# Kernel tuning notes

Measured on AMD Instinct MI355X. Metric: run time of the kernel, lower is better.

The kernel has to match this reference:

```python
import jax, jax.numpy as jnp
import numpy as np

LAYER_SIZES = [1024, 1024, 1024, 1024, 1024, 1024, 512]
MAX_PATHS = 128
BATCH = 128
N_LAYERS = len(LAYER_SIZES) - 1


def setup_inputs() -> dict:
    key = jax.random.key(0)
    keys = jax.random.split(key, 1 + 2 * N_LAYERS)
    inp = {"x": jax.random.normal(keys[0], (BATCH, LAYER_SIZES[0]), dtype=jnp.float32)}
    for i in range(N_LAYERS):
        inp[f"W{i}"] = jax.random.normal(keys[1 + 2 * i], (LAYER_SIZES[i], LAYER_SIZES[i + 1]), dtype=jnp.float32) * 0.01
        inp[f"b{i}"] = jax.random.normal(keys[2 + 2 * i], (LAYER_SIZES[i + 1],), dtype=jnp.float32) * 0.01
    return inp


def _layer(data, W, b):
    # data: [B, in_feat, P] -> [B, out_feat, 3P]
    B, _, P = data.shape
    O = W.shape[1]
    pos = jnp.einsum('bfp,fo->bpo', data, W) + b          # [B, P, O]; neg branch is exactly -pos
    branches = jnp.stack([-pos, jnp.zeros_like(pos), pos], axis=-1)  # [B, P, O, 3]
    # transpose(1,2) then reshape: interleave branches per source path, matching torch
    return branches.transpose(0, 2, 1, 3).reshape(B, O, P * 3)


def _prune(data, keep):
    # keep top-`keep` paths by L2 norm over the feature dim
    norms = jnp.linalg.norm(data, axis=1)                 # [B, P]
    _, idx = jax.lax.top_k(norms, keep)                   # [B, keep]
    return jnp.take_along_axis(data, idx[:, None, :], axis=-1)


def _forward(x, Ws, bs):
    data = x[:, :, None]                                   # [B, F, 1]
    for i in range(N_LAYERS):
        data = _layer(data, Ws[i], bs[i])
        if i < N_LAYERS - 1:
            data = jnp.tanh(data)
        if data.shape[-1] > MAX_PATHS:
            data = _prune(data, MAX_PATHS)
    # collapse with 'max_abs': per (batch, feature) pick path with largest |value|
    idx = jnp.argmax(jnp.abs(data), axis=-1, keepdims=True)
    output = jnp.take_along_axis(data, idx, axis=-1).squeeze(-1)
    return output, data


def reference(x, W0, b0, W1, b1, W2, b2, W3, b3, W4, b4, W5, b5):
    Ws = [W0, W1, W2, W3, W4, W5]
    bs = [b0, b1, b2, b3, b4, b5]
    return _forward(x, Ws, bs)
```

## Files before the change

### kernel.cpp

```cpp
#include <hip/hip_runtime.h>
#include <math.h>


using s8v = __attribute__((ext_vector_type(8))) short;
using f4v = __attribute__((ext_vector_type(4))) float;

__device__ __forceinline__ float bf2f(short b) {
  unsigned u = ((unsigned)(unsigned short)b) << 16;
  return __builtin_bit_cast(float, u);
}
__device__ __forceinline__ short f2bf(float f) {
  unsigned u = __builtin_bit_cast(unsigned, f);
  u = (u + 0x7FFFu + ((u >> 16) & 1u)) >> 16;
  return (short)u;
}
__device__ __forceinline__ void split_store(float f, short* hi, short* lo) {
  short h = f2bf(f);
  *hi = h;
  *lo = f2bf(f - bf2f(h));
}

struct TWArgs {
  const float* W[6];
  short* Th[6];
  short* Tl[6];
};
__global__ void __launch_bounds__(256)
transW_all(TWArgs a, const float* __restrict__ x, short* __restrict__ A0h,
           short* __restrict__ A0l) {
  __shared__ float tile[64][65];
  const int t = threadIdx.x;
  if (blockIdx.z == 6) {
    const int bf = blockIdx.y * 16 + blockIdx.x;
    if (bf < 128) {
      int i = (bf * 256 + t) * 4;
      float4 v = *(const float4*)&x[i];
      short4 h, l;
      h.x = f2bf(v.x); l.x = f2bf(v.x - bf2f(h.x));
      h.y = f2bf(v.y); l.y = f2bf(v.y - bf2f(h.y));
      h.z = f2bf(v.z); l.z = f2bf(v.z - bf2f(h.z));
      h.w = f2bf(v.w); l.w = f2bf(v.w - bf2f(h.w));
      *(short4*)&A0h[i] = h;
      *(short4*)&A0l[i] = l;
    }
    return;
  }
  const int z = blockIdx.z;
  const int N = (z == 5) ? 512 : 1024;
  const int n0 = blockIdx.x * 64, k0 = blockIdx.y * 64;
  if (n0 >= N) return;
  const float* __restrict__ W = a.W[z];
  short* __restrict__ Th = a.Th[z];
  short* __restrict__ Tl = a.Tl[z];
  const int r = t >> 4, c4 = (t & 15) * 4;
#pragma unroll
  for (int i = 0; i < 4; ++i) {
    int rr = r + 16 * i;
    float4 v = *(const float4*)&W[(size_t)(k0 + rr) * N + n0 + c4];
    tile[rr][c4 + 0] = v.x;
    tile[rr][c4 + 1] = v.y;
    tile[rr][c4 + 2] = v.z;
    tile[rr][c4 + 3] = v.w;
  }
  __syncthreads();
#pragma unroll
  for (int i = 0; i < 4; ++i) {
    int n = r + 16 * i;
    short4 h, l;
    float f0 = tile[c4 + 0][n], f1 = tile[c4 + 1][n];
    float f2 = tile[c4 + 2][n], f3 = tile[c4 + 3][n];
    h.x = f2bf(f0); l.x = f2bf(f0 - bf2f(h.x));
    h.y = f2bf(f1); l.y = f2bf(f1 - bf2f(h.y));
    h.z = f2bf(f2); l.z = f2bf(f2 - bf2f(h.z));
    h.w = f2bf(f3); l.w = f2bf(f3 - bf2f(h.w));
    size_t o = (size_t)(n0 + n) * 1024 + k0 + c4;
    *(short4*)&Th[o] = h;
    *(short4*)&Tl[o] = l;
  }
}

template <int MODE, int D, int KS>
__global__ void __launch_bounds__(256, 2)
mfma_gemm(const short* __restrict__ Ah, const short* __restrict__ Al,
          const short* __restrict__ Bh, const short* __restrict__ Bl,
          const float* __restrict__ bias, short* __restrict__ Oh,
          short* __restrict__ Ol, float* __restrict__ Of, int N, int Dn) {
  constexpr int KC = 1024 / KS;
  constexpr int BKP = 40;
  __shared__ short As_h[64 * BKP], As_l[64 * BKP];
  __shared__ short Bs_h[64 * BKP], Bs_l[64 * BKP];
  const int t = threadIdx.x;
  const int row0 = blockIdx.y * 64;
  const int col0 = blockIdx.x * 64;
  const int kb = blockIdx.z * KC;
  const int sr = t >> 2, sko = (t & 3) * 8;
  const short* Ahp = Ah + (size_t)(row0 + sr) * 1024 + kb + sko;
  const short* Alp = Al + (size_t)(row0 + sr) * 1024 + kb + sko;
  const short* Bhp = Bh + (size_t)(col0 + sr) * 1024 + kb + sko;
  const short* Blp = Bl + (size_t)(col0 + sr) * 1024 + kb + sko;
  const int w = t >> 6, lane = t & 63;
  const int l16 = lane & 15, q = lane >> 4;
  const int wm0 = (w & 1) * 32, wn0 = (w >> 1) * 32;
  const int abase = (wm0 + l16) * BKP + q * 8;
  const int bbase = (wn0 + l16) * BKP + q * 8;
  f4v acc[2][2];
#pragma unroll
  for (int i = 0; i < 2; ++i)
#pragma unroll
    for (int j = 0; j < 2; ++j) acc[i][j] = (f4v){0.f, 0.f, 0.f, 0.f};
  uint4 rah = *(const uint4*)(Ahp);
  uint4 ral = *(const uint4*)(Alp);
  uint4 rbh = *(const uint4*)(Bhp);
  uint4 rbl = *(const uint4*)(Blp);
  for (int k0 = 0; k0 < KC; k0 += 32) {
    __syncthreads();
    *(uint4*)&As_h[sr * BKP + sko] = rah;
    *(uint4*)&As_l[sr * BKP + sko] = ral;
    *(uint4*)&Bs_h[sr * BKP + sko] = rbh;
    *(uint4*)&Bs_l[sr * BKP + sko] = rbl;
    if (k0 + 32 < KC) {
      rah = *(const uint4*)(Ahp + k0 + 32);
      ral = *(const uint4*)(Alp + k0 + 32);
      rbh = *(const uint4*)(Bhp + k0 + 32);
      rbl = *(const uint4*)(Blp + k0 + 32);
    }
    __syncthreads();
    s8v ah[2], al[2], bh[2], bl[2];
#pragma unroll
    for (int mt = 0; mt < 2; ++mt) {
      ah[mt] = *(const s8v*)&As_h[abase + mt * 16 * BKP];
      al[mt] = *(const s8v*)&As_l[abase + mt * 16 * BKP];
    }
#pragma unroll
    for (int nt = 0; nt < 2; ++nt) {
      bh[nt] = *(const s8v*)&Bs_h[bbase + nt * 16 * BKP];
      bl[nt] = *(const s8v*)&Bs_l[bbase + nt * 16 * BKP];
    }
#pragma unroll
    for (int mt = 0; mt < 2; ++mt)
#pragma unroll
      for (int nt = 0; nt < 2; ++nt) {
        acc[mt][nt] = __builtin_amdgcn_mfma_f32_16x16x32_bf16(
            ah[mt], bh[nt], acc[mt][nt], 0, 0, 0);
        acc[mt][nt] = __builtin_amdgcn_mfma_f32_16x16x32_bf16(
            ah[mt], bl[nt], acc[mt][nt], 0, 0, 0);
        acc[mt][nt] = __builtin_amdgcn_mfma_f32_16x16x32_bf16(
            al[mt], bh[nt], acc[mt][nt], 0, 0, 0);
      }
  }
  const int R = (int)gridDim.y << 6;
#pragma unroll
  for (int nt = 0; nt < 2; ++nt) {
    int gcol = col0 + wn0 + nt * 16 + l16;
    float bc = (MODE == 1) ? bias[gcol] : 0.f;
#pragma unroll
    for (int mt = 0; mt < 2; ++mt) {
#pragma unroll
      for (int r = 0; r < 4; ++r) {
        float v = acc[mt][nt][r];
        int rr = row0 + wm0 + mt * 16 + q * 4 + r;
        if (MODE == 1) {
          int b = rr / D, u = rr - b * D;
          size_t ob = (size_t)(b * Dn) * N + gcol;
          size_t om = ob + (size_t)(1 + 2 * u) * N;
          size_t op = ob + (size_t)(2 + 2 * u) * N;
          split_store(tanhf(bc - v), &Oh[om], &Ol[om]);
          split_store(tanhf(bc + v), &Oh[op], &Ol[op]);
          if (u == 0) split_store(tanhf(bc), &Oh[ob], &Ol[ob]);
        } else if (MODE == 2) {
          Of[(size_t)rr * N + gcol] = v;
        } else {
          Of[((size_t)blockIdx.z * R + rr) * N + gcol] = v;
        }
      }
    }
  }
}

template <int KS>
__global__ void __launch_bounds__(256)
comb0_hl(const float* __restrict__ P, const float* __restrict__ bias,
         short* __restrict__ Oh, short* __restrict__ Ol, int R, int N) {
  int i = blockIdx.x * 256 + threadIdx.x;
  int n4 = N >> 2;
  int r = i / n4, c4 = (i - r * n4) * 4;
  float4 y = *(const float4*)&P[(size_t)r * N + c4];
  size_t stride = (size_t)R * N;
#pragma unroll
  for (int ks = 1; ks < KS; ++ks) {
    const float4 p = *(const float4*)&P[ks * stride + (size_t)r * N + c4];
    y.x += p.x; y.y += p.y; y.z += p.z; y.w += p.w;
  }
  float4 bc = *(const float4*)(bias + c4);
  float t0 = tanhf(bc.x + y.x), t1 = tanhf(bc.y + y.y);
  float t2 = tanhf(bc.z + y.z), t3 = tanhf(bc.w + y.w);
  short4 h, l;
  h.x = f2bf(t0); l.x = f2bf(t0 - bf2f(h.x));
  h.y = f2bf(t1); l.y = f2bf(t1 - bf2f(h.y));
  h.z = f2bf(t2); l.z = f2bf(t2 - bf2f(h.z));
  h.w = f2bf(t3); l.w = f2bf(t3 - bf2f(h.w));
  *(short4*)&Oh[(size_t)r * N + c4] = h;
  *(short4*)&Ol[(size_t)r * N + c4] = l;
}

template <int KS, int D>
__global__ void __launch_bounds__(256)
comb1_hl(const float* __restrict__ P, const float* __restrict__ bias,
         short* __restrict__ Oh, short* __restrict__ Ol, int R, int N,
         int Dn) {
  int i = blockIdx.x * 256 + threadIdx.x;
  int n4 = N >> 2;
  int r = i / n4, c4 = (i - r * n4) * 4;
  int b = r / D, u = r - b * D;
  float4 y = *(const float4*)&P[(size_t)r * N + c4];
  size_t stride = (size_t)R * N;
#pragma unroll
  for (int ks = 1; ks < KS; ++ks) {
    const float4 p = *(const float4*)&P[ks * stride + (size_t)r * N + c4];
    y.x += p.x; y.y += p.y; y.z += p.z; y.w += p.w;
  }
  float4 bc = *(const float4*)(bias + c4);
  size_t ob = (size_t)(b * Dn) * N + c4;
  size_t om = ob + (size_t)(1 + 2 * u) * N;
  size_t op = ob + (size_t)(2 + 2 * u) * N;
  {
    float t0 = tanhf(bc.x - y.x), t1 = tanhf(bc.y - y.y);
    float t2 = tanhf(bc.z - y.z), t3 = tanhf(bc.w - y.w);
    short4 h, l;
    h.x = f2bf(t0); l.x = f2bf(t0 - bf2f(h.x));
    h.y = f2bf(t1); l.y = f2bf(t1 - bf2f(h.y));
    h.z = f2bf(t2); l.z = f2bf(t2 - bf2f(h.z));
    h.w = f2bf(t3); l.w = f2bf(t3 - bf2f(h.w));
    *(short4*)&Oh[om] = h;
    *(short4*)&Ol[om] = l;
  }
  {
    float t0 = tanhf(bc.x + y.x), t1 = tanhf(bc.y + y.y);
    float t2 = tanhf(bc.z + y.z), t3 = tanhf(bc.w + y.w);
    short4 h, l;
    h.x = f2bf(t0); l.x = f2bf(t0 - bf2f(h.x));
    h.y = f2bf(t1); l.y = f2bf(t1 - bf2f(h.y));
    h.z = f2bf(t2); l.z = f2bf(t2 - bf2f(h.z));
    h.w = f2bf(t3); l.w = f2bf(t3 - bf2f(h.w));
    *(short4*)&Oh[op] = h;
    *(short4*)&Ol[op] = l;
  }
  if (u == 0) {
    float t0 = tanhf(bc.x), t1 = tanhf(bc.y);
    float t2 = tanhf(bc.z), t3 = tanhf(bc.w);
    short4 h, l;
    h.x = f2bf(t0); l.x = f2bf(t0 - bf2f(h.x));
    h.y = f2bf(t1); l.y = f2bf(t1 - bf2f(h.y));
    h.z = f2bf(t2); l.z = f2bf(t2 - bf2f(h.z));
    h.w = f2bf(t3); l.w = f2bf(t3 - bf2f(h.w));
    *(short4*)&Oh[ob] = h;
    *(short4*)&Ol[ob] = l;
  }
}

__global__ void __launch_bounds__(256)
rownorm_hl(const short* __restrict__ hi, const short* __restrict__ lo,
           float* __restrict__ ns) {
  int row = blockIdx.x;
  int t = threadIdx.x;
  size_t base = (size_t)row * 1024 + t * 4;
  short4 h = *(const short4*)&hi[base];
  short4 l = *(const short4*)&lo[base];
  float v0 = bf2f(h.x) + bf2f(l.x);
  float v1 = bf2f(h.y) + bf2f(l.y);
  float v2 = bf2f(h.z) + bf2f(l.z);
  float v3 = bf2f(h.w) + bf2f(l.w);
  float s = v0 * v0 + v1 * v1 + v2 * v2 + v3 * v3;
  __shared__ float red[256];
  red[t] = s;
  __syncthreads();
  for (int off = 128; off; off >>= 1) {
    if (t < off) red[t] += red[t + off];
    __syncthreads();
  }
  if (t == 0) ns[row] = red[0];
}

__global__ void __launch_bounds__(256)
stats5_k(const float* __restrict__ Y5, const float* __restrict__ b5,
         float* __restrict__ dotv, float* __restrict__ nrmv) {
  int row = blockIdx.x;
  int t = threadIdx.x;
  __shared__ float rd[256], rn[256];
  const float* y = Y5 + (size_t)row * 512;
  float d = 0.f, n2 = 0.f;
  for (int o = t; o < 512; o += 256) {
    float v = y[o];
    d = fmaf(b5[o], v, d);
    n2 = fmaf(v, v, n2);
  }
  rd[t] = d;
  rn[t] = n2;
  __syncthreads();
  for (int off = 128; off; off >>= 1) {
    if (t < off) {
      rd[t] += rd[t + off];
      rn[t] += rn[t + off];
    }
    __syncthreads();
  }
  if (t == 0) {
    dotv[row] = rd[0];
    nrmv[row] = rn[0];
  }
}

__global__ void __launch_bounds__(384)
prune45_k(const float* __restrict__ ns, const float* __restrict__ dotv,
          const float* __restrict__ nrmv, const float* __restrict__ b5,
          int* __restrict__ kept4, int* __restrict__ kept5) {
  const int b = blockIdx.x, t = threadIdx.x;
  __shared__ float nss[31];
  __shared__ float rb[256];
  __shared__ float keyA[243];
  __shared__ int cls[243];
  __shared__ int k4s[128];
  __shared__ float pns[128];
  __shared__ float keyB[384];
  if (t < 31) nss[t] = ns[b * 31 + t];
  if (t < 256) {
    float a = b5[t], c = b5[t + 256];
    rb[t] = fmaf(a, a, 0.f);
    rb[t] = fmaf(c, c, rb[t]);
  }
  __syncthreads();
  for (int off = 128; off; off >>= 1) {
    if (t < off) rb[t] += rb[t + off];
    __syncthreads();
  }
  const float nb5 = rb[0];
  if (t < 243) {
    int j = t / 3, t4 = t - 3 * j;
    int d0 = j / 27, d1 = (j / 9) % 3, d2 = (j / 3) % 3, d3 = j % 3;
    int u = 0;
    u = (d0 == 1) ? 0 : (1 + 2 * u + (d0 == 2));
    u = (d1 == 1) ? 0 : (1 + 2 * u + (d1 == 2));
    u = (d2 == 1) ? 0 : (1 + 2 * u + (d2 == 2));
    u = (d3 == 1) ? 0 : (1 + 2 * u + (d3 == 2));
    cls[t] = u;
    keyA[t] = (t4 == 1) ? 0.f : nss[u];
  }
  __syncthreads();
  if (t < 243) {
    float k = keyA[t];
    int rank = 0;
    for (int e = 0; e < 243; ++e) {
      float ke = keyA[e];
      rank += (ke > k) || (ke == k && e < t);
    }
    if (rank < 128) {
      int t4 = t - 3 * (t / 3);
      int kv = (cls[t] << 1) | (t4 == 2 ? 1 : 0);
      k4s[rank] = kv;
      kept4[b * 128 + rank] = kv;
    }
  }
  __syncthreads();
  if (t < 128) {
    int k4 = k4s[t];
    int c = k4 >> 1;
    float s = (k4 & 1) ? 1.f : -1.f;
    pns[t] = nb5 + nrmv[b * 31 + c] + s * 2.f * dotv[b * 31 + c];
  }
  __syncthreads();
  const int m = t / 3, tt = t - 3 * m;
  keyB[t] = (tt == 1) ? 0.f : pns[m];
  __syncthreads();
  float k = keyB[t];
  int rank = 0;
  for (int e = 0; e < 384; ++e) {
    float ke = keyB[e];
    rank += (ke > k) || (ke == k && e < t);
  }
  if (rank < 128) kept5[b * 128 + rank] = (m << 1) | (tt == 2 ? 1 : 0);
}

__global__ void __launch_bounds__(256)
finalize_k(const float* __restrict__ Y5, const float* __restrict__ b5,
           const int* __restrict__ kept4, const int* __restrict__ kept5,
           float* __restrict__ out, float* __restrict__ dataout) {
  const int b = blockIdx.y;
  const int o0 = blockIdx.x * 64;
  __shared__ float Ys[31][65];
  __shared__ float bias_s[64];
  __shared__ float vt[64][130];
  __shared__ float ra[64][4];
  __shared__ float rv[64][4];
  const int t = threadIdx.x;
  for (int idx = t; idx < 31 * 64; idx += 256) {
    int c = idx >> 6, o = idx & 63;
    Ys[c][o] = Y5[((size_t)b * 31 + c) * 512 + o0 + o];
  }
  if (t < 64) bias_s[t] = b5[o0 + t];
  const int rr = t & 127, oh = t >> 7;
  int k5 = kept5[b * 128 + rr];
  int m = k5 >> 1;
  float sig = (k5 & 1) ? 1.f : -1.f;
  int k4 = kept4[b * 128 + m];
  int cc = k4 >> 1;
  float s4 = (k4 & 1) ? 1.f : -1.f;
  float afac = sig * s4;
  __syncthreads();
#pragma unroll
  for (int ol = 0; ol < 32; ++ol) {
    int o = oh * 32 + ol;
    float v = sig * bias_s[o] + afac * Ys[cc][o];
    dataout[((size_t)b * 512 + o0 + o) * 128 + rr] = v;
    vt[o][rr] = v;
  }
  __syncthreads();
  int o = t >> 2, q = t & 3;
  float bestv = vt[o][q * 32];
  float besta = fabsf(bestv);
  for (int i = 1; i < 32; ++i) {
    float v = vt[o][q * 32 + i];
    float a = fabsf(v);
    if (a > besta) {
      besta = a;
      bestv = v;
    }
  }
  ra[o][q] = besta;
  rv[o][q] = bestv;
  __syncthreads();
  if (t < 64) {
    float ba = ra[t][0], bv = rv[t][0];
#pragma unroll
    for (int qq = 1; qq < 4; ++qq) {
      if (ra[t][qq] > ba) {
        ba = ra[t][qq];
        bv = rv[t][qq];
      }
    }
    out[(size_t)b * 512 + o0 + t] = bv;
  }
}

extern "C" void kernel_launch(void* const* d_in, const int* in_sizes, int n_in,
                              void* d_out, int out_size, void* d_ws,
                              size_t ws_size, hipStream_t stream) {
  const float* x = (const float*)d_in[0];
  const float* Wt[6];
  const float* bs[6];
  for (int i = 0; i < 6; ++i) {
    Wt[i] = (const float*)d_in[1 + 2 * i];
    bs[i] = (const float*)d_in[2 + 2 * i];
  }
  char* base = (char*)d_ws;
  short* A0h = (short*)(base + 0);
  short* A0l = (short*)(base + 262144);
  short* Wh[6], *Wl[6];
  {
    size_t off = 524288;
    for (int i = 0; i < 6; ++i) {
      size_t sz = (i < 5) ? 2097152 : 1048576;
      Wh[i] = (short*)(base + off);
      Wl[i] = (short*)(base + off + sz);
      off += 2 * sz;
    }
  }
  short* C1h = (short*)(base + 23592960), *C1l = (short*)(base + 23855104);
  short* C2h = (short*)(base + 24117248), *C2l = (short*)(base + 24903680);
  short* C3h = (short*)(base + 25690112), *C3l = (short*)(base + 27525120);
  short* C4h = (short*)(base + 29360128), *C4l = (short*)(base + 33292288);
  short* C5h = (short*)(base + 524288);
  short* C5l = (short*)(base + 8912896);
  float* PA = (float*)(base + 29360128);
  float* PB = (float*)(base + 524288);
  float* Y5 = (float*)(base + 23592960);
  float* ns = (float*)(base + 37224448);
  float* dotv = (float*)(base + 37240320);
  float* nrmv = (float*)(base + 37256192);
  int* kept4 = (int*)(base + 37272068);
  int* kept5 = (int*)(base + 37337604);
  float* outp = (float*)d_out;
  float* dataout = outp + 128 * 512;

  dim3 blk(256);
  TWArgs twa;
  for (int i = 0; i < 6; ++i) {
    twa.W[i] = Wt[i];
    twa.Th[i] = Wh[i];
    twa.Tl[i] = Wl[i];
  }
  transW_all<<<dim3(16, 16, 7), blk, 0, stream>>>(twa, x, A0h, A0l);
  mfma_gemm<3, 1, 4><<<dim3(16, 2, 4), blk, 0, stream>>>(
      A0h, A0l, Wh[0], Wl[0], nullptr, nullptr, nullptr, PA, 1024, 0);
  comb0_hl<4><<<dim3(128), blk, 0, stream>>>(PA, bs[0], C1h, C1l, 128, 1024);
  mfma_gemm<3, 1, 4><<<dim3(16, 2, 4), blk, 0, stream>>>(
      C1h, C1l, Wh[1], Wl[1], nullptr, nullptr, nullptr, PA, 1024, 0);
  comb1_hl<4, 1><<<dim3(128), blk, 0, stream>>>(PA, bs[1], C2h, C2l, 128, 1024,
                                                3);
  mfma_gemm<3, 3, 4><<<dim3(16, 6, 4), blk, 0, stream>>>(
      C2h, C2l, Wh[2], Wl[2], nullptr, nullptr, nullptr, PA, 1024, 0);
  comb1_hl<4, 3><<<dim3(384), blk, 0, stream>>>(PA, bs[2], C3h, C3l, 384, 1024,
                                                7);
  mfma_gemm<3, 7, 2><<<dim3(16, 14, 2), blk, 0, stream>>>(
      C3h, C3l, Wh[3], Wl[3], nullptr, nullptr, nullptr, PB, 1024, 0);
  comb1_hl<2, 7><<<dim3(896), blk, 0, stream>>>(PB, bs[3], C4h, C4l, 896, 1024,
                                                15);
  mfma_gemm<1, 15, 1><<<dim3(16, 30), blk, 0, stream>>>(
      C4h, C4l, Wh[4], Wl[4], bs[4], C5h, C5l, nullptr, 1024, 31);
  rownorm_hl<<<dim3(3968), blk, 0, stream>>>(C5h, C5l, ns);
  mfma_gemm<2, 31, 1><<<dim3(8, 62), blk, 0, stream>>>(
      C5h, C5l, Wh[5], Wl[5], nullptr, nullptr, nullptr, Y5, 512, 0);
  stats5_k<<<dim3(3968), blk, 0, stream>>>(Y5, bs[5], dotv, nrmv);
  prune45_k<<<dim3(128), dim3(384), 0, stream>>>(ns, dotv, nrmv, bs[5], kept4,
                                                 kept5);
  finalize_k<<<dim3(8, 128), blk, 0, stream>>>(Y5, bs[5], kept4, kept5, outp,
                                               dataout);
}
```

Before: 238.5 us.

## Double GEMM K-step to 64 and fuse layer-5 GEMM with row-norm kernel

The MFMA GEMM now stages 64 K-elements per shared-memory iteration instead of 32 (padded row stride raised to 72), which halves the number of barrier pairs per K loop but doubles register prefetch and LDS footprint. The GEMM body is factored into a device function so the final-layer GEMM and the row-norm reduction can run as one launch. Blocks below 496 do the GEMM and the rest compute row norms, which removes a kernel launch and lets the two independent jobs overlap. The larger LDS use per block may lower occupancy, and the row-norm blocks now inherit the GEMM's launch bounds and shared-memory allocation.

```diff
diff --git a/kernel.cpp b/kernel.cpp
--- a/kernel.cpp
+++ b/kernel.cpp
@@ -80,19 +80,20 @@
 }
 
 template <int MODE, int D, int KS>
-__global__ void __launch_bounds__(256, 2)
-mfma_gemm(const short* __restrict__ Ah, const short* __restrict__ Al,
-          const short* __restrict__ Bh, const short* __restrict__ Bl,
-          const float* __restrict__ bias, short* __restrict__ Oh,
-          short* __restrict__ Ol, float* __restrict__ Of, int N, int Dn) {
+__device__ __forceinline__ void gemm_body(
+    int bx, int by, int bz, int R, const short* __restrict__ Ah,
+    const short* __restrict__ Al, const short* __restrict__ Bh,
+    const short* __restrict__ Bl, const float* __restrict__ bias,
+    short* __restrict__ Oh, short* __restrict__ Ol, float* __restrict__ Of,
+    int N, int Dn) {
   constexpr int KC = 1024 / KS;
-  constexpr int BKP = 40;
+  constexpr int BKP = 72;
   __shared__ short As_h[64 * BKP], As_l[64 * BKP];
   __shared__ short Bs_h[64 * BKP], Bs_l[64 * BKP];
   const int t = threadIdx.x;
-  const int row0 = blockIdx.y * 64;
-  const int col0 = blockIdx.x * 64;
-  const int kb = blockIdx.z * KC;
+  const int row0 = by * 64;
+  const int col0 = bx * 64;
+  const int kb = bz * KC;
   const int sr = t >> 2, sko = (t & 3) * 8;
   const short* Ahp = Ah + (size_t)(row0 + sr) * 1024 + kb + sko;
   const short* Alp = Al + (size_t)(row0 + sr) * 1024 + kb + sko;
@@ -108,47 +109,59 @@
   for (int i = 0; i < 2; ++i)
 #pragma unroll
     for (int j = 0; j < 2; ++j) acc[i][j] = (f4v){0.f, 0.f, 0.f, 0.f};
-  uint4 rah = *(const uint4*)(Ahp);
-  uint4 ral = *(const uint4*)(Alp);
-  uint4 rbh = *(const uint4*)(Bhp);
-  uint4 rbl = *(const uint4*)(Blp);
-  for (int k0 = 0; k0 < KC; k0 += 32) {
+  uint4 rah[2], ral[2], rbh[2], rbl[2];
+#pragma unroll
+  for (int c = 0; c < 2; ++c) {
+    rah[c] = *(const uint4*)(Ahp + c * 32);
+    ral[c] = *(const uint4*)(Alp + c * 32);
+    rbh[c] = *(const uint4*)(Bhp + c * 32);
+    rbl[c] = *(const uint4*)(Blp + c * 32);
+  }
+  for (int k0 = 0; k0 < KC; k0 += 64) {
     __syncthreads();
-    *(uint4*)&As_h[sr * BKP + sko] = rah;
-    *(uint4*)&As_l[sr * BKP + sko] = ral;
-    *(uint4*)&Bs_h[sr * BKP + sko] = rbh;
-    *(uint4*)&Bs_l[sr * BKP + sko] = rbl;
-    if (k0 + 32 < KC) {
-      rah = *(const uint4*)(Ahp + k0 + 32);
-      ral = *(const uint4*)(Alp + k0 + 32);
-      rbh = *(const uint4*)(Bhp + k0 + 32);
-      rbl = *(const uint4*)(Blp + k0 + 32);
+#pragma unroll
+    for (int c = 0; c < 2; ++c) {
+      *(uint4*)&As_h[sr * BKP + sko + c * 32] = rah[c];
+      *(uint4*)&As_l[sr * BKP + sko + c * 32] = ral[c];
+      *(uint4*)&Bs_h[sr * BKP + sko + c * 32] = rbh[c];
+      *(uint4*)&Bs_l[sr * BKP + sko + c * 32] = rbl[c];
+    }
+    if (k0 + 64 < KC) {
+#pragma unroll
+      for (int c = 0; c < 2; ++c) {
+        rah[c] = *(const uint4*)(Ahp + k0 + 64 + c * 32);
+        ral[c] = *(const uint4*)(Alp + k0 + 64 + c * 32);
+        rbh[c] = *(const uint4*)(Bhp + k0 + 64 + c * 32);
+        rbl[c] = *(const uint4*)(Blp + k0 + 64 + c * 32);
+      }
     }
     __syncthreads();
-    s8v ah[2], al[2], bh[2], bl[2];
-#pragma unroll
-    for (int mt = 0; mt < 2; ++mt) {
-      ah[mt] = *(const s8v*)&As_h[abase + mt * 16 * BKP];
-      al[mt] = *(const s8v*)&As_l[abase + mt * 16 * BKP];
-    }
-#pragma unroll
-    for (int nt = 0; nt < 2; ++nt) {
-      bh[nt] = *(const s8v*)&Bs_h[bbase + nt * 16 * BKP];
-      bl[nt] = *(const s8v*)&Bs_l[bbase + nt * 16 * BKP];
-    }
-#pragma unroll
-    for (int mt = 0; mt < 2; ++mt)
+#pragma unroll
+    for (int kk = 0; kk < 64; kk += 32) {
+      s8v ah[2], al[2], bh[2], bl[2];
+#pragma unroll
+      for (int mt = 0; mt < 2; ++mt) {
+        ah[mt] = *(const s8v*)&As_h[abase + mt * 16 * BKP + kk];
+        al[mt] = *(const s8v*)&As_l[abase + mt * 16 * BKP + kk];
+      }
 #pragma unroll
       for (int nt = 0; nt < 2; ++nt) {
-        acc[mt][nt] = __builtin_amdgcn_mfma_f32_16x16x32_bf16(
-            ah[mt], bh[nt], acc[mt][nt], 0, 0, 0);
-        acc[mt][nt] = __builtin_amdgcn_mfma_f32_16x16x32_bf16(
-            ah[mt], bl[nt], acc[mt][nt], 0, 0, 0);
-        acc[mt][nt] = __builtin_amdgcn_mfma_f32_16x16x32_bf16(
-            al[mt], bh[nt], acc[mt][nt], 0, 0, 0);
+        bh[nt] = *(const s8v*)&Bs_h[bbase + nt * 16 * BKP + kk];
+        bl[nt] = *(const s8v*)&Bs_l[bbase + nt * 16 * BKP + kk];
       }
-  }
-  const int R = (int)gridDim.y << 6;
+#pragma unroll
+      for (int mt = 0; mt < 2; ++mt)
+#pragma unroll
+        for (int nt = 0; nt < 2; ++nt) {
+          acc[mt][nt] = __builtin_amdgcn_mfma_f32_16x16x32_bf16(
+              ah[mt], bh[nt], acc[mt][nt], 0, 0, 0);
+          acc[mt][nt] = __builtin_amdgcn_mfma_f32_16x16x32_bf16(
+              ah[mt], bl[nt], acc[mt][nt], 0, 0, 0);
+          acc[mt][nt] = __builtin_amdgcn_mfma_f32_16x16x32_bf16(
+              al[mt], bh[nt], acc[mt][nt], 0, 0, 0);
+        }
+    }
+  }
 #pragma unroll
   for (int nt = 0; nt < 2; ++nt) {
     int gcol = col0 + wn0 + nt * 16 + l16;
@@ -170,10 +183,56 @@
         } else if (MODE == 2) {
           Of[(size_t)rr * N + gcol] = v;
         } else {
-          Of[((size_t)blockIdx.z * R + rr) * N + gcol] = v;
+          Of[((size_t)bz * R + rr) * N + gcol] = v;
         }
       }
     }
+  }
+}
+
+template <int MODE, int D, int KS>
+__global__ void __launch_bounds__(256, 2)
+mfma_gemm(const short* __restrict__ Ah, const short* __restrict__ Al,
+          const short* __restrict__ Bh, const short* __restrict__ Bl,
+          const float* __restrict__ bias, short* __restrict__ Oh,
+          short* __restrict__ Ol, float* __restrict__ Of, int N, int Dn) {
+  gemm_body<MODE, D, KS>(blockIdx.x, blockIdx.y, blockIdx.z,
+                         (int)gridDim.y << 6, Ah, Al, Bh, Bl, bias, Oh, Ol,
+                         Of, N, Dn);
+}
+
+__device__ __forceinline__ void rownorm_body(const short* __restrict__ hi,
+                                             const short* __restrict__ lo,
+                                             float* __restrict__ ns, int row) {
+  int t = threadIdx.x;
+  size_t base = (size_t)row * 1024 + t * 4;
+  short4 h = *(const short4*)&hi[base];
+  short4 l = *(const short4*)&lo[base];
+  float v0 = bf2f(h.x) + bf2f(l.x);
+  float v1 = bf2f(h.y) + bf2f(l.y);
+  float v2 = bf2f(h.z) + bf2f(l.z);
+  float v3 = bf2f(h.w) + bf2f(l.w);
+  float s = v0 * v0 + v1 * v1 + v2 * v2 + v3 * v3;
+  __shared__ float red[256];
+  red[t] = s;
+  __syncthreads();
+  for (int off = 128; off; off >>= 1) {
+    if (t < off) red[t] += red[t + off];
+    __syncthreads();
+  }
+  if (t == 0) ns[row] = red[0];
+}
+
+__global__ void __launch_bounds__(256, 2)
+gemm5_rownorm(const short* __restrict__ C5h, const short* __restrict__ C5l,
+              const short* __restrict__ W5h, const short* __restrict__ W5l,
+              float* __restrict__ Y5, float* __restrict__ ns) {
+  const int bid = blockIdx.x;
+  if (bid < 496) {
+    gemm_body<2, 31, 1>(bid & 7, bid >> 3, 0, 0, C5h, C5l, W5h, W5l, nullptr,
+                        nullptr, nullptr, Y5, 512, 0);
+  } else {
+    rownorm_body(C5h, C5l, ns, bid - 496);
   }
 }
 
@@ -256,29 +315,6 @@
     *(short4*)&Oh[ob] = h;
     *(short4*)&Ol[ob] = l;
   }
-}
-
-__global__ void __launch_bounds__(256)
-rownorm_hl(const short* __restrict__ hi, const short* __restrict__ lo,
-           float* __restrict__ ns) {
-  int row = blockIdx.x;
-  int t = threadIdx.x;
-  size_t base = (size_t)row * 1024 + t * 4;
-  short4 h = *(const short4*)&hi[base];
-  short4 l = *(const short4*)&lo[base];
-  float v0 = bf2f(h.x) + bf2f(l.x);
-  float v1 = bf2f(h.y) + bf2f(l.y);
-  float v2 = bf2f(h.z) + bf2f(l.z);
-  float v3 = bf2f(h.w) + bf2f(l.w);
-  float s = v0 * v0 + v1 * v1 + v2 * v2 + v3 * v3;
-  __shared__ float red[256];
-  red[t] = s;
-  __syncthreads();
-  for (int off = 128; off; off >>= 1) {
-    if (t < off) red[t] += red[t + off];
-    __syncthreads();
-  }
-  if (t == 0) ns[row] = red[0];
 }
 
 __global__ void __launch_bounds__(256)
@@ -506,9 +542,8 @@
                                                 15);
   mfma_gemm<1, 15, 1><<<dim3(16, 30), blk, 0, stream>>>(
       C4h, C4l, Wh[4], Wl[4], bs[4], C5h, C5l, nullptr, 1024, 31);
-  rownorm_hl<<<dim3(3968), blk, 0, stream>>>(C5h, C5l, ns);
-  mfma_gemm<2, 31, 1><<<dim3(8, 62), blk, 0, stream>>>(
-      C5h, C5l, Wh[5], Wl[5], nullptr, nullptr, nullptr, Y5, 512, 0);
+  gemm5_rownorm<<<dim3(496 + 3968), blk, 0, stream>>>(C5h, C5l, Wh[5], Wl[5],
+                                                      Y5, ns);
   stats5_k<<<dim3(3968), blk, 0, stream>>>(Y5, bs[5], dotv, nrmv);
   prune45_k<<<dim3(128), dim3(384), 0, stream>>>(ns, dotv, nrmv, bs[5], kept4,
                                                  kept5);
```

After: 397.2 us. +66.5%, slower.

## Halve GEMM row tile to 32 and fuse final GEMM with row-norm kernel

Applied to the files above, without the earlier changes.

Shrinks the MFMA GEMM block tile from 64x64 to 32x64, so each wave computes a 32x16 strip. Grid y-dimensions double, giving more blocks for these small-M GEMMs to fill the CUs. A-tile loading is split so half the threads load the hi part and half the lo part. The last GEMM and the row-norm reduction are merged into one launch that branches on block id, which removes a launch and lets the two independent jobs run concurrently. The cost is less B-tile reuse per block and more total global traffic for B.

```diff
diff --git a/kernel.cpp b/kernel.cpp
--- a/kernel.cpp
+++ b/kernel.cpp
@@ -80,85 +80,76 @@
 }
 
 template <int MODE, int D, int KS>
-__global__ void __launch_bounds__(256, 2)
-mfma_gemm(const short* __restrict__ Ah, const short* __restrict__ Al,
-          const short* __restrict__ Bh, const short* __restrict__ Bl,
-          const float* __restrict__ bias, short* __restrict__ Oh,
-          short* __restrict__ Ol, float* __restrict__ Of, int N, int Dn) {
+__device__ __forceinline__ void gemm_body(
+    int bx, int by, int bz, int R, const short* __restrict__ Ah,
+    const short* __restrict__ Al, const short* __restrict__ Bh,
+    const short* __restrict__ Bl, const float* __restrict__ bias,
+    short* __restrict__ Oh, short* __restrict__ Ol, float* __restrict__ Of,
+    int N, int Dn) {
   constexpr int KC = 1024 / KS;
   constexpr int BKP = 40;
-  __shared__ short As_h[64 * BKP], As_l[64 * BKP];
+  __shared__ short As_h[32 * BKP], As_l[32 * BKP];
   __shared__ short Bs_h[64 * BKP], Bs_l[64 * BKP];
   const int t = threadIdx.x;
-  const int row0 = blockIdx.y * 64;
-  const int col0 = blockIdx.x * 64;
-  const int kb = blockIdx.z * KC;
+  const int row0 = by * 32;
+  const int col0 = bx * 64;
+  const int kb = bz * KC;
   const int sr = t >> 2, sko = (t & 3) * 8;
-  const short* Ahp = Ah + (size_t)(row0 + sr) * 1024 + kb + sko;
-  const short* Alp = Al + (size_t)(row0 + sr) * 1024 + kb + sko;
   const short* Bhp = Bh + (size_t)(col0 + sr) * 1024 + kb + sko;
   const short* Blp = Bl + (size_t)(col0 + sr) * 1024 + kb + sko;
+  const int ta = t & 127;
+  const int ar = ta >> 2, ako = (ta & 3) * 8;
+  const short* Ap = (t < 128 ? Ah : Al) + (size_t)(row0 + ar) * 1024 + kb + ako;
+  short* AsDst = (t < 128) ? As_h : As_l;
   const int w = t >> 6, lane = t & 63;
   const int l16 = lane & 15, q = lane >> 4;
-  const int wm0 = (w & 1) * 32, wn0 = (w >> 1) * 32;
-  const int abase = (wm0 + l16) * BKP + q * 8;
+  const int wn0 = w * 16;
+  const int abase = l16 * BKP + q * 8;
   const int bbase = (wn0 + l16) * BKP + q * 8;
-  f4v acc[2][2];
-#pragma unroll
-  for (int i = 0; i < 2; ++i)
-#pragma unroll
-    for (int j = 0; j < 2; ++j) acc[i][j] = (f4v){0.f, 0.f, 0.f, 0.f};
-  uint4 rah = *(const uint4*)(Ahp);
-  uint4 ral = *(const uint4*)(Alp);
+  f4v acc[2];
+#pragma unroll
+  for (int i = 0; i < 2; ++i) acc[i] = (f4v){0.f, 0.f, 0.f, 0.f};
+  uint4 ra = *(const uint4*)(Ap);
   uint4 rbh = *(const uint4*)(Bhp);
   uint4 rbl = *(const uint4*)(Blp);
   for (int k0 = 0; k0 < KC; k0 += 32) {
     __syncthreads();
-    *(uint4*)&As_h[sr * BKP + sko] = rah;
-    *(uint4*)&As_l[sr * BKP + sko] = ral;
+    *(uint4*)&AsDst[ar * BKP + ako] = ra;
     *(uint4*)&Bs_h[sr * BKP + sko] = rbh;
     *(uint4*)&Bs_l[sr * BKP + sko] = rbl;
     if (k0 + 32 < KC) {
-      rah = *(const uint4*)(Ahp + k0 + 32);
-      ral = *(const uint4*)(Alp + k0 + 32);
+      ra = *(const uint4*)(Ap + k0 + 32);
       rbh = *(const uint4*)(Bhp + k0 + 32);
       rbl = *(const uint4*)(Blp + k0 + 32);
     }
     __syncthreads();
-    s8v ah[2], al[2], bh[2], bl[2];
+    s8v ah[2], al[2], bh, bl;
 #pragma unroll
     for (int mt = 0; mt < 2; ++mt) {
       ah[mt] = *(const s8v*)&As_h[abase + mt * 16 * BKP];
       al[mt] = *(const s8v*)&As_l[abase + mt * 16 * BKP];
     }
-#pragma unroll
-    for (int nt = 0; nt < 2; ++nt) {
-      bh[nt] = *(const s8v*)&Bs_h[bbase + nt * 16 * BKP];
-      bl[nt] = *(const s8v*)&Bs_l[bbase + nt * 16 * BKP];
-    }
-#pragma unroll
-    for (int mt = 0; mt < 2; ++mt)
-#pragma unroll
-      for (int nt = 0; nt < 2; ++nt) {
-        acc[mt][nt] = __builtin_amdgcn_mfma_f32_16x16x32_bf16(
-            ah[mt], bh[nt], acc[mt][nt], 0, 0, 0);
-        acc[mt][nt] = __builtin_amdgcn_mfma_f32_16x16x32_bf16(
-            ah[mt], bl[nt], acc[mt][nt], 0, 0, 0);
-        acc[mt][nt] = __builtin_amdgcn_mfma_f32_16x16x32_bf16(
-            al[mt], bh[nt], acc[mt][nt], 0, 0, 0);
-      }
-  }
-  const int R = (int)gridDim.y << 6;
-#pragma unroll
-  for (int nt = 0; nt < 2; ++nt) {
-    int gcol = col0 + wn0 + nt * 16 + l16;
+    bh = *(const s8v*)&Bs_h[bbase];
+    bl = *(const s8v*)&Bs_l[bbase];
+#pragma unroll
+    for (int mt = 0; mt < 2; ++mt) {
+      acc[mt] = __builtin_amdgcn_mfma_f32_16x16x32_bf16(ah[mt], bh, acc[mt],
+                                                        0, 0, 0);
+      acc[mt] = __builtin_amdgcn_mfma_f32_16x16x32_bf16(ah[mt], bl, acc[mt],
+                                                        0, 0, 0);
+      acc[mt] = __builtin_amdgcn_mfma_f32_16x16x32_bf16(al[mt], bh, acc[mt],
+                                                        0, 0, 0);
+    }
+  }
+  {
+    int gcol = col0 + wn0 + l16;
     float bc = (MODE == 1) ? bias[gcol] : 0.f;
 #pragma unroll
     for (int mt = 0; mt < 2; ++mt) {
 #pragma unroll
       for (int r = 0; r < 4; ++r) {
-        float v = acc[mt][nt][r];
-        int rr = row0 + wm0 + mt * 16 + q * 4 + r;
+        float v = acc[mt][r];
+        int rr = row0 + mt * 16 + q * 4 + r;
         if (MODE == 1) {
           int b = rr / D, u = rr - b * D;
           size_t ob = (size_t)(b * Dn) * N + gcol;
@@ -170,10 +161,56 @@
         } else if (MODE == 2) {
           Of[(size_t)rr * N + gcol] = v;
         } else {
-          Of[((size_t)blockIdx.z * R + rr) * N + gcol] = v;
+          Of[((size_t)bz * R + rr) * N + gcol] = v;
         }
       }
     }
+  }
+}
+
+template <int MODE, int D, int KS>
+__global__ void __launch_bounds__(256, 2)
+mfma_gemm(const short* __restrict__ Ah, const short* __restrict__ Al,
+          const short* __restrict__ Bh, const short* __restrict__ Bl,
+          const float* __restrict__ bias, short* __restrict__ Oh,
+          short* __restrict__ Ol, float* __restrict__ Of, int N, int Dn) {
+  gemm_body<MODE, D, KS>(blockIdx.x, blockIdx.y, blockIdx.z,
+                         (int)gridDim.y << 5, Ah, Al, Bh, Bl, bias, Oh, Ol,
+                         Of, N, Dn);
+}
+
+__device__ __forceinline__ void rownorm_body(const short* __restrict__ hi,
+                                             const short* __restrict__ lo,
+                                             float* __restrict__ ns, int row) {
+  int t = threadIdx.x;
+  size_t base = (size_t)row * 1024 + t * 4;
+  short4 h = *(const short4*)&hi[base];
+  short4 l = *(const short4*)&lo[base];
+  float v0 = bf2f(h.x) + bf2f(l.x);
+  float v1 = bf2f(h.y) + bf2f(l.y);
+  float v2 = bf2f(h.z) + bf2f(l.z);
+  float v3 = bf2f(h.w) + bf2f(l.w);
+  float s = v0 * v0 + v1 * v1 + v2 * v2 + v3 * v3;
+  __shared__ float red[256];
+  red[t] = s;
+  __syncthreads();
+  for (int off = 128; off; off >>= 1) {
+    if (t < off) red[t] += red[t + off];
+    __syncthreads();
+  }
+  if (t == 0) ns[row] = red[0];
+}
+
+__global__ void __launch_bounds__(256, 2)
+gemm5_rownorm(const short* __restrict__ C5h, const short* __restrict__ C5l,
+              const short* __restrict__ W5h, const short* __restrict__ W5l,
+              float* __restrict__ Y5, float* __restrict__ ns) {
+  const int bid = blockIdx.x;
+  if (bid < 992) {
+    gemm_body<2, 31, 1>(bid & 7, bid >> 3, 0, 0, C5h, C5l, W5h, W5l, nullptr,
+                        nullptr, nullptr, Y5, 512, 0);
+  } else {
+    rownorm_body(C5h, C5l, ns, bid - 992);
   }
 }
 
@@ -256,29 +293,6 @@
     *(short4*)&Oh[ob] = h;
     *(short4*)&Ol[ob] = l;
   }
-}
-
-__global__ void __launch_bounds__(256)
-rownorm_hl(const short* __restrict__ hi, const short* __restrict__ lo,
-           float* __restrict__ ns) {
-  int row = blockIdx.x;
-  int t = threadIdx.x;
-  size_t base = (size_t)row * 1024 + t * 4;
-  short4 h = *(const short4*)&hi[base];
-  short4 l = *(const short4*)&lo[base];
-  float v0 = bf2f(h.x) + bf2f(l.x);
-  float v1 = bf2f(h.y) + bf2f(l.y);
-  float v2 = bf2f(h.z) + bf2f(l.z);
-  float v3 = bf2f(h.w) + bf2f(l.w);
-  float s = v0 * v0 + v1 * v1 + v2 * v2 + v3 * v3;
-  __shared__ float red[256];
-  red[t] = s;
-  __syncthreads();
-  for (int off = 128; off; off >>= 1) {
-    if (t < off) red[t] += red[t + off];
-    __syncthreads();
-  }
-  if (t == 0) ns[row] = red[0];
 }
 
 __global__ void __launch_bounds__(256)
@@ -489,26 +503,25 @@
     twa.Tl[i] = Wl[i];
   }
   transW_all<<<dim3(16, 16, 7), blk, 0, stream>>>(twa, x, A0h, A0l);
-  mfma_gemm<3, 1, 4><<<dim3(16, 2, 4), blk, 0, stream>>>(
+  mfma_gemm<3, 1, 4><<<dim3(16, 4, 4), blk, 0, stream>>>(
       A0h, A0l, Wh[0], Wl[0], nullptr, nullptr, nullptr, PA, 1024, 0);
   comb0_hl<4><<<dim3(128), blk, 0, stream>>>(PA, bs[0], C1h, C1l, 128, 1024);
-  mfma_gemm<3, 1, 4><<<dim3(16, 2, 4), blk, 0, stream>>>(
+  mfma_gemm<3, 1, 4><<<dim3(16, 4, 4), blk, 0, stream>>>(
       C1h, C1l, Wh[1], Wl[1], nullptr, nullptr, nullptr, PA, 1024, 0);
   comb1_hl<4, 1><<<dim3(128), blk, 0, stream>>>(PA, bs[1], C2h, C2l, 128, 1024,
                                                 3);
-  mfma_gemm<3, 3, 4><<<dim3(16, 6, 4), blk, 0, stream>>>(
+  mfma_gemm<3, 3, 4><<<dim3(16, 12, 4), blk, 0, stream>>>(
       C2h, C2l, Wh[2], Wl[2], nullptr, nullptr, nullptr, PA, 1024, 0);
   comb1_hl<4, 3><<<dim3(384), blk, 0, stream>>>(PA, bs[2], C3h, C3l, 384, 1024,
                                                 7);
-  mfma_gemm<3, 7, 2><<<dim3(16, 14, 2), blk, 0, stream>>>(
+  mfma_gemm<3, 7, 2><<<dim3(16, 28, 2), blk, 0, stream>>>(
       C3h, C3l, Wh[3], Wl[3], nullptr, nullptr, nullptr, PB, 1024, 0);
   comb1_hl<2, 7><<<dim3(896), blk, 0, stream>>>(PB, bs[3], C4h, C4l, 896, 1024,
                                                 15);
-  mfma_gemm<1, 15, 1><<<dim3(16, 30), blk, 0, stream>>>(
+  mfma_gemm<1, 15, 1><<<dim3(16, 60), blk, 0, stream>>>(
       C4h, C4l, Wh[4], Wl[4], bs[4], C5h, C5l, nullptr, 1024, 31);
-  rownorm_hl<<<dim3(3968), blk, 0, stream>>>(C5h, C5l, ns);
-  mfma_gemm<2, 31, 1><<<dim3(8, 62), blk, 0, stream>>>(
-      C5h, C5l, Wh[5], Wl[5], nullptr, nullptr, nullptr, Y5, 512, 0);
+  gemm5_rownorm<<<dim3(992 + 3968), blk, 0, stream>>>(C5h, C5l, Wh[5], Wl[5],
+                                                      Y5, ns);
   stats5_k<<<dim3(3968), blk, 0, stream>>>(Y5, bs[5], dotv, nrmv);
   prune45_k<<<dim3(128), dim3(384), 0, stream>>>(ns, dotv, nrmv, bs[5], kept4,
                                                  kept5);
```

Result: slower. 251.2 us (+5.3%).

## Fuse rownorm into last GEMM launch and merge prune into finalize

Applied to the files above, without the earlier changes.

The row-norm kernel now runs as extra blocks in the same launch as the final GEMM, so the two independent jobs share one launch. The prune kernel is folded into finalize: each finalize block recomputes the top-k selection for its batch in shared memory instead of reading kept indices from global memory. This removes two launches and a global round-trip, but the prune work is now repeated by all 8 column blocks per batch, and finalize runs 384 threads with more shared memory.

```diff
diff --git a/kernel.cpp b/kernel.cpp
--- a/kernel.cpp
+++ b/kernel.cpp
@@ -80,19 +80,20 @@
 }
 
 template <int MODE, int D, int KS>
-__global__ void __launch_bounds__(256, 2)
-mfma_gemm(const short* __restrict__ Ah, const short* __restrict__ Al,
-          const short* __restrict__ Bh, const short* __restrict__ Bl,
-          const float* __restrict__ bias, short* __restrict__ Oh,
-          short* __restrict__ Ol, float* __restrict__ Of, int N, int Dn) {
+__device__ __forceinline__ void gemm_body(
+    int bx, int by, int bz, int R, const short* __restrict__ Ah,
+    const short* __restrict__ Al, const short* __restrict__ Bh,
+    const short* __restrict__ Bl, const float* __restrict__ bias,
+    short* __restrict__ Oh, short* __restrict__ Ol, float* __restrict__ Of,
+    int N, int Dn) {
   constexpr int KC = 1024 / KS;
   constexpr int BKP = 40;
   __shared__ short As_h[64 * BKP], As_l[64 * BKP];
   __shared__ short Bs_h[64 * BKP], Bs_l[64 * BKP];
   const int t = threadIdx.x;
-  const int row0 = blockIdx.y * 64;
-  const int col0 = blockIdx.x * 64;
-  const int kb = blockIdx.z * KC;
+  const int row0 = by * 64;
+  const int col0 = bx * 64;
+  const int kb = bz * KC;
   const int sr = t >> 2, sko = (t & 3) * 8;
   const short* Ahp = Ah + (size_t)(row0 + sr) * 1024 + kb + sko;
   const short* Alp = Al + (size_t)(row0 + sr) * 1024 + kb + sko;
@@ -148,7 +149,6 @@
             al[mt], bh[nt], acc[mt][nt], 0, 0, 0);
       }
   }
-  const int R = (int)gridDim.y << 6;
 #pragma unroll
   for (int nt = 0; nt < 2; ++nt) {
     int gcol = col0 + wn0 + nt * 16 + l16;
@@ -170,10 +170,56 @@
         } else if (MODE == 2) {
           Of[(size_t)rr * N + gcol] = v;
         } else {
-          Of[((size_t)blockIdx.z * R + rr) * N + gcol] = v;
+          Of[((size_t)bz * R + rr) * N + gcol] = v;
         }
       }
     }
+  }
+}
+
+template <int MODE, int D, int KS>
+__global__ void __launch_bounds__(256, 2)
+mfma_gemm(const short* __restrict__ Ah, const short* __restrict__ Al,
+          const short* __restrict__ Bh, const short* __restrict__ Bl,
+          const float* __restrict__ bias, short* __restrict__ Oh,
+          short* __restrict__ Ol, float* __restrict__ Of, int N, int Dn) {
+  gemm_body<MODE, D, KS>(blockIdx.x, blockIdx.y, blockIdx.z,
+                         (int)gridDim.y << 6, Ah, Al, Bh, Bl, bias, Oh, Ol,
+                         Of, N, Dn);
+}
+
+__device__ __forceinline__ void rownorm_body(const short* __restrict__ hi,
+                                             const short* __restrict__ lo,
+                                             float* __restrict__ ns, int row) {
+  int t = threadIdx.x;
+  size_t base = (size_t)row * 1024 + t * 4;
+  short4 h = *(const short4*)&hi[base];
+  short4 l = *(const short4*)&lo[base];
+  float v0 = bf2f(h.x) + bf2f(l.x);
+  float v1 = bf2f(h.y) + bf2f(l.y);
+  float v2 = bf2f(h.z) + bf2f(l.z);
+  float v3 = bf2f(h.w) + bf2f(l.w);
+  float s = v0 * v0 + v1 * v1 + v2 * v2 + v3 * v3;
+  __shared__ float red[256];
+  red[t] = s;
+  __syncthreads();
+  for (int off = 128; off; off >>= 1) {
+    if (t < off) red[t] += red[t + off];
+    __syncthreads();
+  }
+  if (t == 0) ns[row] = red[0];
+}
+
+__global__ void __launch_bounds__(256, 2)
+gemm5_rownorm(const short* __restrict__ C5h, const short* __restrict__ C5l,
+              const short* __restrict__ W5h, const short* __restrict__ W5l,
+              float* __restrict__ Y5, float* __restrict__ ns) {
+  const int bid = blockIdx.x;
+  if (bid < 496) {
+    gemm_body<2, 31, 1>(bid & 7, bid >> 3, 0, 0, C5h, C5l, W5h, W5l, nullptr,
+                        nullptr, nullptr, Y5, 512, 0);
+  } else {
+    rownorm_body(C5h, C5l, ns, bid - 496);
   }
 }
 
@@ -259,29 +305,6 @@
 }
 
 __global__ void __launch_bounds__(256)
-rownorm_hl(const short* __restrict__ hi, const short* __restrict__ lo,
-           float* __restrict__ ns) {
-  int row = blockIdx.x;
-  int t = threadIdx.x;
-  size_t base = (size_t)row * 1024 + t * 4;
-  short4 h = *(const short4*)&hi[base];
-  short4 l = *(const short4*)&lo[base];
-  float v0 = bf2f(h.x) + bf2f(l.x);
-  float v1 = bf2f(h.y) + bf2f(l.y);
-  float v2 = bf2f(h.z) + bf2f(l.z);
-  float v3 = bf2f(h.w) + bf2f(l.w);
-  float s = v0 * v0 + v1 * v1 + v2 * v2 + v3 * v3;
-  __shared__ float red[256];
-  red[t] = s;
-  __syncthreads();
-  for (int off = 128; off; off >>= 1) {
-    if (t < off) red[t] += red[t + off];
-    __syncthreads();
-  }
-  if (t == 0) ns[row] = red[0];
-}
-
-__global__ void __launch_bounds__(256)
 stats5_k(const float* __restrict__ Y5, const float* __restrict__ b5,
          float* __restrict__ dotv, float* __restrict__ nrmv) {
   int row = blockIdx.x;
@@ -311,10 +334,12 @@
 }
 
 __global__ void __launch_bounds__(384)
-prune45_k(const float* __restrict__ ns, const float* __restrict__ dotv,
-          const float* __restrict__ nrmv, const float* __restrict__ b5,
-          int* __restrict__ kept4, int* __restrict__ kept5) {
-  const int b = blockIdx.x, t = threadIdx.x;
+finalize_k(const float* __restrict__ Y5, const float* __restrict__ b5,
+           const float* __restrict__ ns, const float* __restrict__ dotv,
+           const float* __restrict__ nrmv, float* __restrict__ out,
+           float* __restrict__ dataout) {
+  const int b = blockIdx.y;
+  const int o0 = blockIdx.x * 64;
   __shared__ float nss[31];
   __shared__ float rb[256];
   __shared__ float keyA[243];
@@ -322,6 +347,18 @@
   __shared__ int k4s[128];
   __shared__ float pns[128];
   __shared__ float keyB[384];
+  __shared__ int k5s[128];
+  __shared__ float Ys[31][65];
+  __shared__ float bias_s[64];
+  __shared__ float vt[64][130];
+  __shared__ float ra[64][4];
+  __shared__ float rv[64][4];
+  const int t = threadIdx.x;
+  for (int idx = t; idx < 31 * 64; idx += 384) {
+    int c = idx >> 6, o = idx & 63;
+    Ys[c][o] = Y5[((size_t)b * 31 + c) * 512 + o0 + o];
+  }
+  if (t < 64) bias_s[t] = b5[o0 + t];
   if (t < 31) nss[t] = ns[b * 31 + t];
   if (t < 256) {
     float a = b5[t], c = b5[t + 256];
@@ -355,9 +392,7 @@
     }
     if (rank < 128) {
       int t4 = t - 3 * (t / 3);
-      int kv = (cls[t] << 1) | (t4 == 2 ? 1 : 0);
-      k4s[rank] = kv;
-      kept4[b * 128 + rank] = kv;
+      k4s[rank] = (cls[t] << 1) | (t4 == 2 ? 1 : 0);
     }
   }
   __syncthreads();
@@ -368,65 +403,52 @@
     pns[t] = nb5 + nrmv[b * 31 + c] + s * 2.f * dotv[b * 31 + c];
   }
   __syncthreads();
-  const int m = t / 3, tt = t - 3 * m;
-  keyB[t] = (tt == 1) ? 0.f : pns[m];
-  __syncthreads();
-  float k = keyB[t];
-  int rank = 0;
-  for (int e = 0; e < 384; ++e) {
-    float ke = keyB[e];
-    rank += (ke > k) || (ke == k && e < t);
-  }
-  if (rank < 128) kept5[b * 128 + rank] = (m << 1) | (tt == 2 ? 1 : 0);
-}
-
-__global__ void __launch_bounds__(256)
-finalize_k(const float* __restrict__ Y5, const float* __restrict__ b5,
-           const int* __restrict__ kept4, const int* __restrict__ kept5,
-           float* __restrict__ out, float* __restrict__ dataout) {
-  const int b = blockIdx.y;
-  const int o0 = blockIdx.x * 64;
-  __shared__ float Ys[31][65];
-  __shared__ float bias_s[64];
-  __shared__ float vt[64][130];
-  __shared__ float ra[64][4];
-  __shared__ float rv[64][4];
-  const int t = threadIdx.x;
-  for (int idx = t; idx < 31 * 64; idx += 256) {
-    int c = idx >> 6, o = idx & 63;
-    Ys[c][o] = Y5[((size_t)b * 31 + c) * 512 + o0 + o];
-  }
-  if (t < 64) bias_s[t] = b5[o0 + t];
-  const int rr = t & 127, oh = t >> 7;
-  int k5 = kept5[b * 128 + rr];
-  int m = k5 >> 1;
-  float sig = (k5 & 1) ? 1.f : -1.f;
-  int k4 = kept4[b * 128 + m];
-  int cc = k4 >> 1;
-  float s4 = (k4 & 1) ? 1.f : -1.f;
-  float afac = sig * s4;
-  __syncthreads();
-#pragma unroll
-  for (int ol = 0; ol < 32; ++ol) {
-    int o = oh * 32 + ol;
-    float v = sig * bias_s[o] + afac * Ys[cc][o];
-    dataout[((size_t)b * 512 + o0 + o) * 128 + rr] = v;
-    vt[o][rr] = v;
-  }
-  __syncthreads();
-  int o = t >> 2, q = t & 3;
-  float bestv = vt[o][q * 32];
-  float besta = fabsf(bestv);
-  for (int i = 1; i < 32; ++i) {
-    float v = vt[o][q * 32 + i];
-    float a = fabsf(v);
-    if (a > besta) {
-      besta = a;
-      bestv = v;
-    }
-  }
-  ra[o][q] = besta;
-  rv[o][q] = bestv;
+  {
+    const int m = t / 3, tt = t - 3 * m;
+    keyB[t] = (tt == 1) ? 0.f : pns[m];
+    __syncthreads();
+    float k = keyB[t];
+    int rank = 0;
+    for (int e = 0; e < 384; ++e) {
+      float ke = keyB[e];
+      rank += (ke > k) || (ke == k && e < t);
+    }
+    if (rank < 128) k5s[rank] = (m << 1) | (tt == 2 ? 1 : 0);
+  }
+  __syncthreads();
+  if (t < 256) {
+    const int rr = t & 127, oh = t >> 7;
+    int k5 = k5s[rr];
+    int m = k5 >> 1;
+    float sig = (k5 & 1) ? 1.f : -1.f;
+    int k4 = k4s[m];
+    int cc = k4 >> 1;
+    float s4 = (k4 & 1) ? 1.f : -1.f;
+    float afac = sig * s4;
+#pragma unroll
+    for (int ol = 0; ol < 32; ++ol) {
+      int o = oh * 32 + ol;
+      float v = sig * bias_s[o] + afac * Ys[cc][o];
+      dataout[((size_t)b * 512 + o0 + o) * 128 + rr] = v;
+      vt[o][rr] = v;
+    }
+  }
+  __syncthreads();
+  if (t < 256) {
+    int o = t >> 2, q = t & 3;
+    float bestv = vt[o][q * 32];
+    float besta = fabsf(bestv);
+    for (int i = 1; i < 32; ++i) {
+      float v = vt[o][q * 32 + i];
+      float a = fabsf(v);
+      if (a > besta) {
+        besta = a;
+        bestv = v;
+      }
+    }
+    ra[o][q] = besta;
+    rv[o][q] = bestv;
+  }
   __syncthreads();
   if (t < 64) {
     float ba = ra[t][0], bv = rv[t][0];
@@ -476,8 +498,6 @@
   float* ns = (float*)(base + 37224448);
   float* dotv = (float*)(base + 37240320);
   float* nrmv = (float*)(base + 37256192);
-  int* kept4 = (int*)(base + 37272068);
-  int* kept5 = (int*)(base + 37337604);
   float* outp = (float*)d_out;
   float* dataout = outp + 128 * 512;
 
@@ -506,12 +526,9 @@
                                                 15);
   mfma_gemm<1, 15, 1><<<dim3(16, 30), blk, 0, stream>>>(
       C4h, C4l, Wh[4], Wl[4], bs[4], C5h, C5l, nullptr, 1024, 31);
-  rownorm_hl<<<dim3(3968), blk, 0, stream>>>(C5h, C5l, ns);
-  mfma_gemm<2, 31, 1><<<dim3(8, 62), blk, 0, stream>>>(
-      C5h, C5l, Wh[5], Wl[5], nullptr, nullptr, nullptr, Y5, 512, 0);
+  gemm5_rownorm<<<dim3(496 + 3968), blk, 0, stream>>>(C5h, C5l, Wh[5], Wl[5],
+                                                      Y5, ns);
   stats5_k<<<dim3(3968), blk, 0, stream>>>(Y5, bs[5], dotv, nrmv);
-  prune45_k<<<dim3(128), dim3(384), 0, stream>>>(ns, dotv, nrmv, bs[5], kept4,
-                                                 kept5);
-  finalize_k<<<dim3(8, 128), blk, 0, stream>>>(Y5, bs[5], kept4, kept5, outp,
-                                               dataout);
-}
+  finalize_k<<<dim3(8, 128), dim3(384), 0, stream>>>(Y5, bs[5], ns, dotv,
+                                                     nrmv, outp, dataout);
+}
```

Result: slower. 264.2 us (+10.8%).
